# Kernel optimization log

Hardware: AMD Instinct MI355X
Metric: run time of the kernel (lower is better)

The kernel has to match this reference:

```python
import jax, jax.numpy as jnp
import numpy as np

N, D = 8192, 512


def setup_inputs() -> dict:
    key = jax.random.key(0)
    ks = jax.random.split(key, 4)
    scale = 1.0 / np.sqrt(D)
    x = jax.random.normal(ks[0], (N, D), dtype=jnp.float32)
    Wq = jax.random.normal(ks[1], (D, D), dtype=jnp.float32) * scale
    Wk = jax.random.normal(ks[2], (D, D), dtype=jnp.float32) * scale
    Wv = jax.random.normal(ks[3], (D, D), dtype=jnp.float32) * scale
    bq = jnp.zeros((D,), dtype=jnp.float32)
    bk = jnp.zeros((D,), dtype=jnp.float32)
    bv = jnp.zeros((D,), dtype=jnp.float32)
    # causal additive mask: 0 on/below diagonal, -1e9 above
    mask = jnp.where(jnp.arange(N)[:, None] >= jnp.arange(N)[None, :], 0.0, -1e9).astype(jnp.float32)
    return {"x": x, "mask": mask, "Wq": Wq, "bq": bq, "Wk": Wk, "bk": bk, "Wv": Wv, "bv": bv}


def reference(x, mask, Wq, bq, Wk, bk, Wv, bv):
    # torch Linear: y = x @ W.T + b
    q = x @ Wq.T + bq  # [N, D]
    k = x @ Wk.T + bk  # [N, D]
    v = x @ Wv.T + bv  # [N, D]
    inv_sqrt_d = 1.0 / jnp.sqrt(jnp.asarray(D, dtype=x.dtype))
    scores = q @ k.T * inv_sqrt_d + mask          # [N, N] -- the HBM-heavy intermediate
    attention = jax.nn.softmax(scores, axis=-1)   # softmax over key axis
    weighted = attention @ v                       # [N, D]
    return weighted
```

## Files before the change

kernel.cpp:

```cpp
#include <hip/hip_runtime.h>
#include <hip/hip_bf16.h>
#include <stdint.h>


#define N_TOK 8192
#define DIM   512
#define NQB   128
#define CCH   12
#define MAXCH 11
#define NCHTOT 748

typedef __attribute__((ext_vector_type(8))) short bfrag;
typedef __attribute__((ext_vector_type(4))) float facc;
typedef __attribute__((ext_vector_type(4))) unsigned short us4v;
typedef __attribute__((ext_vector_type(2))) float f32x2v;

#define MFMA16(a, b, c) __builtin_amdgcn_mfma_f32_16x16x32_bf16((a), (b), (c), 0, 0, 0)

__device__ __forceinline__ unsigned short f2bf(float f) {
    union { float f; unsigned int u; } v; v.f = f;
    unsigned int r = v.u + 0x7fffu + ((v.u >> 16) & 1u);
    return (unsigned short)(r >> 16);
}
__device__ __forceinline__ float bf2f(unsigned int bits16) {
    union { unsigned int u; float f; } v; v.u = bits16 << 16;
    return v.f;
}
__device__ __forceinline__ void cp16(const unsigned short* g, const unsigned short* l) {
    __builtin_amdgcn_global_load_lds(
        (const __attribute__((address_space(1))) void*)g,
        (__attribute__((address_space(3))) void*)l, 16, 0, 0);
}

__device__ __forceinline__ int part_idx(int qb, int c) {
    return qb + 122 * c - 6 * c * c;
}

__global__ void cvt_x_kernel(const float* __restrict__ src,
                             unsigned short* __restrict__ dst, int n4) {
    int i = blockIdx.x * blockDim.x + threadIdx.x;
    if (i >= n4) return;
    float4 v = ((const float4*)src)[i];
    us4v o; o[0] = f2bf(v.x); o[1] = f2bf(v.y); o[2] = f2bf(v.z); o[3] = f2bf(v.w);
    ((us4v*)dst)[i] = o;
}

__global__ void cvt_w_kernel(const float* __restrict__ wq,
                             const float* __restrict__ wk,
                             const float* __restrict__ wv,
                             unsigned short* __restrict__ dst) {
    int i = blockIdx.x * blockDim.x + threadIdx.x;
    int g = i >> 16;
    int o = i & 65535;
    const float* s = (g == 0) ? wq : (g == 1) ? wk : wv;
    float4 v = ((const float4*)s)[o];
    us4v p; p[0] = f2bf(v.x); p[1] = f2bf(v.y); p[2] = f2bf(v.z); p[3] = f2bf(v.w);
    ((us4v*)dst)[i] = p;
}

__global__ __launch_bounds__(512, 1) void qkv_fused(
    const unsigned short* __restrict__ xb,
    const unsigned short* __restrict__ wb,
    const float* __restrict__ biasq, const float* __restrict__ biask,
    const float* __restrict__ biasv,
    unsigned short* __restrict__ Qb, unsigned short* __restrict__ Kb,
    unsigned short* __restrict__ VTb) {
    const int bid = blockIdx.x;
    const int idx = (bid & 7) * 32 + (bid >> 3);
    const int bx = idx >> 2, by = idx & 3;
    const int r0 = bx * 128, c0 = by * 128;
    const int tid = threadIdx.x, lane = tid & 63, w = tid >> 6;
    const int wm = w >> 2, wn = w & 3;
    const int lr = lane & 15, lkc = lane >> 4;

    __shared__ unsigned short A_lds[2][128 * 64];
    __shared__ unsigned short B_lds[2][3][128 * 64];

    const int st_row = w * 8 + (lane >> 3);
    const int st_gs  = ((lane & 7) ^ (lane >> 3)) * 8;
    auto stage = [&](int step, int buf) {
        const int kb = step * 64;
#pragma unroll
        for (int i = 0; i < 2; ++i) {
            const int r = i * 64 + st_row;
            cp16(xb + (size_t)(r0 + r) * 512 + kb + st_gs,
                 &A_lds[buf][(i * 512 + w * 64) * 8]);
#pragma unroll
            for (int z = 0; z < 3; ++z)
                cp16(wb + (size_t)z * 262144 + (size_t)(c0 + r) * 512 + kb + st_gs,
                     &B_lds[buf][z][(i * 512 + w * 64) * 8]);
        }
    };

    facc acc[3][4][2] = {};
    stage(0, 0);
    __syncthreads();

    int buf = 0;
    for (int step = 0; step < 8; ++step) {
        if (step + 1 < 8) stage(step + 1, buf ^ 1);
        bfrag af[4][2];
#pragma unroll
        for (int i = 0; i < 4; ++i) {
            const int m = wm * 64 + i * 16 + lr;
            const int m7 = m & 7;
#pragma unroll
            for (int kk = 0; kk < 2; ++kk)
                af[i][kk] = *(const bfrag*)&A_lds[buf][(m * 8 + ((kk * 4 + lkc) ^ m7)) * 8];
        }
#pragma unroll
        for (int z = 0; z < 3; ++z) {
            bfrag bf[2][2];
#pragma unroll
            for (int j = 0; j < 2; ++j) {
                const int n = wn * 32 + j * 16 + lr;
                const int n7 = n & 7;
#pragma unroll
                for (int kk = 0; kk < 2; ++kk)
                    bf[j][kk] = *(const bfrag*)&B_lds[buf][z][(n * 8 + ((kk * 4 + lkc) ^ n7)) * 8];
            }
            __builtin_amdgcn_s_setprio(1);
#pragma unroll
            for (int kk = 0; kk < 2; ++kk)
#pragma unroll
                for (int i = 0; i < 4; ++i)
#pragma unroll
                    for (int j = 0; j < 2; ++j)
                        acc[z][i][j] = MFMA16(af[i][kk], bf[j][kk], acc[z][i][j]);
            __builtin_amdgcn_s_setprio(0);
        }
        __syncthreads();
        buf ^= 1;
    }

#pragma unroll
    for (int z = 0; z < 3; ++z) {
        const float* bias = (z == 0) ? biasq : (z == 1) ? biask : biasv;
        if (z < 2) {
            unsigned short* out = (z == 0) ? Qb : Kb;
#pragma unroll
            for (int i = 0; i < 4; ++i)
#pragma unroll
                for (int j = 0; j < 2; ++j) {
                    const int col = c0 + wn * 32 + j * 16 + lr;
                    const float bv_ = bias[col];
#pragma unroll
                    for (int r = 0; r < 4; ++r) {
                        const int row = r0 + wm * 64 + i * 16 + lkc * 4 + r;
                        out[(size_t)row * 512 + col] = f2bf(acc[z][i][j][r] + bv_);
                    }
                }
        } else {
#pragma unroll
            for (int i = 0; i < 4; ++i)
#pragma unroll
                for (int j = 0; j < 2; ++j) {
                    const int col = c0 + wn * 32 + j * 16 + lr;
                    const float bv_ = bias[col];
                    us4v pk;
#pragma unroll
                    for (int r = 0; r < 4; ++r) pk[r] = f2bf(acc[z][i][j][r] + bv_);
                    *(us4v*)(VTb + (size_t)col * 8192 + (r0 + wm * 64 + i * 16 + lkc * 4)) = pk;
                }
        }
    }
}

__global__ __launch_bounds__(512, 2) void attn_partial(
    const unsigned short* __restrict__ Qb, const unsigned short* __restrict__ Kb,
    const unsigned short* __restrict__ VTb,
    unsigned short* __restrict__ Opart, float* __restrict__ ml) {
    const int hb   = blockIdx.x;
    const int xcd  = hb & 7, pos = hb >> 3;
    const int idx  = (xcd < 4 ? xcd * 94 : 376 + (xcd - 4) * 93) + pos;
    int c = 0;
#pragma unroll
    for (int cc = 1; cc < MAXCH; ++cc)
        if (idx >= 134 * cc - 6 * cc * cc) c = cc;
    const int qb  = 12 * c + (idx - (134 * c - 6 * c * c));
    const int kb0 = c * CCH;
    const int kb1 = min(kb0 + CCH, qb + 1);

    const int tid  = threadIdx.x;
    const int lane = tid & 63;
    const int wv   = tid >> 6;
    const int sr   = wv & 3;
    const int ch   = wv >> 2;
    const int lr   = lane & 15;
    const int lkc  = lane >> 4;
    const int lk   = lkc * 8;
    const int qrow0 = qb * 64;

    __shared__ unsigned short Klds[2][64 * 512];
    __shared__ float          S_lds[64][65];
    __shared__ unsigned short P_lds[64][80];
    __shared__ float m_lds[64], l_lds[64], sc_lds[64];

    if (tid < 64) { m_lds[tid] = -1e30f; l_lds[tid] = 0.f; }

    auto stage_k = [&](int kb, int buf) {
        const unsigned short* src = Kb + (size_t)kb * (64 * 512) + (lane ^ wv) * 8;
#pragma unroll
        for (int i = 0; i < 8; ++i) {
            const int rl = wv + 8 * i;
            cp16(src + (size_t)rl * 512, &Klds[buf][rl * 512]);
        }
    };

    bfrag q[16];
    {
        const unsigned short* qp = Qb + (size_t)(qrow0 + sr * 16 + lr) * 512 + lk;
#pragma unroll
        for (int s = 0; s < 16; ++s) q[s] = *(const bfrag*)(qp + s * 32);
    }
    facc o[4][4] = {};
    stage_k(kb0, 0);
    __syncthreads();

    const int row = tid >> 3;
    const int sub = tid & 7;
    const float sm_scale = 0.044194173824159216f;
    int cur = 0;

    for (int kb = kb0; kb < kb1; ++kb) {
        const int cb = kb * 64;
        if (kb + 1 < kb1) stage_k(kb + 1, cur ^ 1);
        bfrag vbf[2][4];
#pragma unroll
        for (int s = 0; s < 2; ++s)
#pragma unroll
            for (int j = 0; j < 4; ++j)
                vbf[s][j] = *(const bfrag*)(VTb + (size_t)(wv * 64 + j * 16 + lr) * 8192
                                            + cb + s * 32 + lk);
#pragma unroll
        for (int tc = 0; tc < 2; ++tc) {
            facc sa0 = {}, sa1 = {};
            const int rl = ch * 32 + tc * 16 + lr;
            const unsigned short* kbase = &Klds[cur][rl * 512];
            const int rx = rl & 7;
            __builtin_amdgcn_s_setprio(1);
#pragma unroll
            for (int s = 0; s < 16; s += 2) {
                const int sl0 = (s * 4 + lkc) ^ rx;
                const int sl1 = ((s + 1) * 4 + lkc) ^ rx;
                sa0 = MFMA16(q[s],     *(const bfrag*)(kbase + sl0 * 8), sa0);
                sa1 = MFMA16(q[s + 1], *(const bfrag*)(kbase + sl1 * 8), sa1);
            }
            __builtin_amdgcn_s_setprio(0);
#pragma unroll
            for (int r = 0; r < 4; ++r)
                S_lds[sr * 16 + lkc * 4 + r][ch * 32 + tc * 16 + lr] = sa0[r] + sa1[r];
        }
        __syncthreads();

        {
            const int grow  = qrow0 + row;
            const bool diag = (kb == qb);
            float sv[8];
#pragma unroll
            for (int j = 0; j < 8; ++j) {
                float v = S_lds[row][sub * 8 + j] * sm_scale;
                if (diag && (cb + sub * 8 + j > grow)) v = -1e30f;
                sv[j] = v;
            }
            float mx = sv[0];
#pragma unroll
            for (int j = 1; j < 8; ++j) mx = fmaxf(mx, sv[j]);
            mx = fmaxf(mx, __shfl_xor(mx, 1));
            mx = fmaxf(mx, __shfl_xor(mx, 2));
            mx = fmaxf(mx, __shfl_xor(mx, 4));
            const float m_old = m_lds[row];
            const float m_new = fmaxf(m_old, mx);
            float sum = 0.f;
            bfrag pv_;
#pragma unroll
            for (int j = 0; j < 8; ++j) {
                float p = __expf(sv[j] - m_new);
                sum += p;
                pv_[j] = (short)f2bf(p);
            }
            sum += __shfl_xor(sum, 1);
            sum += __shfl_xor(sum, 2);
            sum += __shfl_xor(sum, 4);
            if (sub == 0) {
                const float scl = __expf(m_old - m_new);
                sc_lds[row] = scl;
                m_lds[row]  = m_new;
                l_lds[row]  = l_lds[row] * scl + sum;
            }
            *(bfrag*)(&P_lds[row][sub * 8]) = pv_;
        }
        __syncthreads();

#pragma unroll
        for (int i = 0; i < 4; ++i) {
            float s0 = sc_lds[i * 16 + lkc * 4 + 0];
            float s1 = sc_lds[i * 16 + lkc * 4 + 1];
            float s2 = sc_lds[i * 16 + lkc * 4 + 2];
            float s3 = sc_lds[i * 16 + lkc * 4 + 3];
#pragma unroll
            for (int j = 0; j < 4; ++j) {
                o[i][j][0] *= s0; o[i][j][1] *= s1;
                o[i][j][2] *= s2; o[i][j][3] *= s3;
            }
        }
#pragma unroll
        for (int s = 0; s < 2; ++s) {
            bfrag pa[4];
#pragma unroll
            for (int i = 0; i < 4; ++i)
                pa[i] = *(const bfrag*)(&P_lds[i * 16 + lr][s * 32 + lk]);
            __builtin_amdgcn_s_setprio(1);
#pragma unroll
            for (int i = 0; i < 4; ++i)
#pragma unroll
                for (int j = 0; j < 4; ++j)
                    o[i][j] = MFMA16(pa[i], vbf[s][j], o[i][j]);
            __builtin_amdgcn_s_setprio(0);
        }
        cur ^= 1;
    }

    {
        const size_t obase = (size_t)idx * (64 * 512);
#pragma unroll
        for (int i = 0; i < 4; ++i)
#pragma unroll
            for (int j = 0; j < 4; ++j) {
                const int colb = wv * 64 + j * 16 + lr;
#pragma unroll
                for (int r = 0; r < 4; ++r) {
                    const int rrow = i * 16 + lkc * 4 + r;
                    Opart[obase + (size_t)rrow * 512 + colb] = f2bf(o[i][j][r]);
                }
            }
        if (tid < 64) {
            ml[(size_t)idx * 128 + tid * 2 + 0] = m_lds[tid];
            ml[(size_t)idx * 128 + tid * 2 + 1] = l_lds[tid];
        }
    }
}

__global__ __launch_bounds__(256) void combine_k(
    const unsigned short* __restrict__ Opart, const float* __restrict__ ml,
    float* __restrict__ out) {
    const int qb  = blockIdx.x;
    const int rg  = blockIdx.y;
    const int nch = qb / 12 + 1;
    const int tid = threadIdx.x;
    __shared__ float wts[MAXCH][8];

    if (tid < 8) {
        const int lrow = rg * 8 + tid;
        float M = -1e30f;
        for (int cc = 0; cc < nch; ++cc)
            M = fmaxf(M, ml[(size_t)part_idx(qb, cc) * 128 + lrow * 2]);
        float den = 0.f;
        for (int cc = 0; cc < nch; ++cc) {
            float mc = ml[(size_t)part_idx(qb, cc) * 128 + lrow * 2];
            float lc = ml[(size_t)part_idx(qb, cc) * 128 + lrow * 2 + 1];
            den += lc * __expf(mc - M);
        }
        const float inv = 1.f / den;
#pragma unroll
        for (int cc = 0; cc < MAXCH; ++cc)
            wts[cc][tid] = (cc < nch)
                ? __expf(ml[(size_t)part_idx(qb, cc) * 128 + lrow * 2] - M) * inv
                : 0.f;
    }
    __syncthreads();

    float a0[8] = {}, a1[8] = {};
#pragma unroll
    for (int cc = 0; cc < MAXCH; ++cc) {
        const size_t base = (size_t)part_idx(qb, cc) * (64 * 512);
#pragma unroll
        for (int r = 0; r < 8; ++r) {
            const unsigned int pk = *(const unsigned int*)(
                Opart + base + (size_t)(rg * 8 + r) * 512 + tid * 2);
            const float w = wts[cc][r];
            a0[r] += w * bf2f(pk & 0xffffu);
            a1[r] += w * bf2f(pk >> 16);
        }
    }
#pragma unroll
    for (int r = 0; r < 8; ++r) {
        f32x2v res; res[0] = a0[r]; res[1] = a1[r];
        *(f32x2v*)(out + (size_t)(qb * 64 + rg * 8 + r) * 512 + tid * 2) = res;
    }
}

extern "C" void kernel_launch(void* const* d_in, const int* in_sizes, int n_in,
                              void* d_out, int out_size, void* d_ws, size_t ws_size,
                              hipStream_t stream) {
    const float* x  = (const float*)d_in[0];
    const float* Wq = (const float*)d_in[2];
    const float* bq = (const float*)d_in[3];
    const float* Wk = (const float*)d_in[4];
    const float* bk = (const float*)d_in[5];
    const float* Wv = (const float*)d_in[6];
    const float* bv = (const float*)d_in[7];
    float* out = (float*)d_out;

    char* ws = (char*)d_ws;
    unsigned short* xb  = (unsigned short*)(ws);
    unsigned short* Wb  = (unsigned short*)(ws + 8388608);
    unsigned short* Qb  = (unsigned short*)(ws + 9961472);
    unsigned short* Kb  = (unsigned short*)(ws + 18350080);
    unsigned short* VTb = (unsigned short*)(ws + 26738688);
    unsigned short* Op  = (unsigned short*)(ws + 35127296);
    float*          mlp = (float*)(ws + 84148224);

    hipLaunchKernelGGL(cvt_x_kernel, dim3(4096), dim3(256), 0, stream, x, xb, 1048576);
    hipLaunchKernelGGL(cvt_w_kernel, dim3(768), dim3(256), 0, stream, Wq, Wk, Wv, Wb);
    hipLaunchKernelGGL(qkv_fused, dim3(256), dim3(512), 0, stream,
                       xb, Wb, bq, bk, bv, Qb, Kb, VTb);
    hipLaunchKernelGGL(attn_partial, dim3(NCHTOT), dim3(512), 0, stream,
                       Qb, Kb, VTb, Op, mlp);
    hipLaunchKernelGGL(combine_k, dim3(NQB, 8), dim3(256), 0, stream, Op, mlp, out);
}
```

Baseline: 518.9 us.

## Replace syncthreads with targeted waitcnt barriers and deepen QKV load pipeline

Swaps __syncthreads for inline-asm barriers that wait only on the needed counters (lgkmcnt or vmcnt), so async global-to-LDS copies can stay in flight across barriers. The QKV GEMM prefetches two stages ahead with a vmcnt(8) wait, and biases are hoisted into registers. The attention kernel issues the next K stage after the V loads, shrinks the P_lds padding and drops the s_setprio hints. The hand-written vmcnt counts and the out-of-range refetch of stage 7 are fragile, and the barriers may let LDS reads race with the in-flight copies.

```diff
diff --git a/kernel.cpp b/kernel.cpp
--- a/kernel.cpp
+++ b/kernel.cpp
@@ -16,6 +16,11 @@
 typedef __attribute__((ext_vector_type(2))) float f32x2v;
 
 #define MFMA16(a, b, c) __builtin_amdgcn_mfma_f32_16x16x32_bf16((a), (b), (c), 0, 0, 0)
+
+#define BAR_LGKM() asm volatile("s_waitcnt lgkmcnt(0)\ns_barrier" ::: "memory")
+#define BAR_VMALL() asm volatile("s_waitcnt vmcnt(0) lgkmcnt(0)\ns_barrier" ::: "memory")
+#define BAR_VM0()  asm volatile("s_waitcnt vmcnt(0)\ns_barrier" ::: "memory")
+#define BAR_VM8()  asm volatile("s_waitcnt vmcnt(8)\ns_barrier" ::: "memory")
 
 __device__ __forceinline__ unsigned short f2bf(float f) {
     union { float f; unsigned int u; } v; v.f = f;
@@ -76,6 +81,15 @@
     __shared__ unsigned short A_lds[2][128 * 64];
     __shared__ unsigned short B_lds[2][3][128 * 64];
 
+    float bias_r[3][2];
+#pragma unroll
+    for (int j = 0; j < 2; ++j) {
+        const int col = c0 + wn * 32 + j * 16 + lr;
+        bias_r[0][j] = biasq[col];
+        bias_r[1][j] = biask[col];
+        bias_r[2][j] = biasv[col];
+    }
+
     const int st_row = w * 8 + (lane >> 3);
     const int st_gs  = ((lane & 7) ^ (lane >> 3)) * 8;
     auto stage = [&](int step, int buf) {
@@ -94,11 +108,11 @@
 
     facc acc[3][4][2] = {};
     stage(0, 0);
-    __syncthreads();
-
-    int buf = 0;
-    for (int step = 0; step < 8; ++step) {
-        if (step + 1 < 8) stage(step + 1, buf ^ 1);
+    stage(1, 1);
+    BAR_VM8();
+
+    for (int t = 0; t < 8; ++t) {
+        const int b = t & 1;
         bfrag af[4][2];
 #pragma unroll
         for (int i = 0; i < 4; ++i) {
@@ -106,7 +120,7 @@
             const int m7 = m & 7;
 #pragma unroll
             for (int kk = 0; kk < 2; ++kk)
-                af[i][kk] = *(const bfrag*)&A_lds[buf][(m * 8 + ((kk * 4 + lkc) ^ m7)) * 8];
+                af[i][kk] = *(const bfrag*)&A_lds[b][(m * 8 + ((kk * 4 + lkc) ^ m7)) * 8];
         }
 #pragma unroll
         for (int z = 0; z < 3; ++z) {
@@ -117,9 +131,8 @@
                 const int n7 = n & 7;
 #pragma unroll
                 for (int kk = 0; kk < 2; ++kk)
-                    bf[j][kk] = *(const bfrag*)&B_lds[buf][z][(n * 8 + ((kk * 4 + lkc) ^ n7)) * 8];
-            }
-            __builtin_amdgcn_s_setprio(1);
+                    bf[j][kk] = *(const bfrag*)&B_lds[b][z][(n * 8 + ((kk * 4 + lkc) ^ n7)) * 8];
+            }
 #pragma unroll
             for (int kk = 0; kk < 2; ++kk)
 #pragma unroll
@@ -127,15 +140,14 @@
 #pragma unroll
                     for (int j = 0; j < 2; ++j)
                         acc[z][i][j] = MFMA16(af[i][kk], bf[j][kk], acc[z][i][j]);
-            __builtin_amdgcn_s_setprio(0);
-        }
-        __syncthreads();
-        buf ^= 1;
+        }
+        BAR_LGKM();
+        stage(min(t + 2, 7), b);
+        BAR_VM8();
     }
 
 #pragma unroll
     for (int z = 0; z < 3; ++z) {
-        const float* bias = (z == 0) ? biasq : (z == 1) ? biask : biasv;
         if (z < 2) {
             unsigned short* out = (z == 0) ? Qb : Kb;
 #pragma unroll
@@ -143,7 +155,7 @@
 #pragma unroll
                 for (int j = 0; j < 2; ++j) {
                     const int col = c0 + wn * 32 + j * 16 + lr;
-                    const float bv_ = bias[col];
+                    const float bv_ = bias_r[z][j];
 #pragma unroll
                     for (int r = 0; r < 4; ++r) {
                         const int row = r0 + wm * 64 + i * 16 + lkc * 4 + r;
@@ -156,7 +168,7 @@
 #pragma unroll
                 for (int j = 0; j < 2; ++j) {
                     const int col = c0 + wn * 32 + j * 16 + lr;
-                    const float bv_ = bias[col];
+                    const float bv_ = bias_r[z][j];
                     us4v pk;
 #pragma unroll
                     for (int r = 0; r < 4; ++r) pk[r] = f2bf(acc[z][i][j][r] + bv_);
@@ -193,7 +205,7 @@
 
     __shared__ unsigned short Klds[2][64 * 512];
     __shared__ float          S_lds[64][65];
-    __shared__ unsigned short P_lds[64][80];
+    __shared__ unsigned short P_lds[64][72];
     __shared__ float m_lds[64], l_lds[64], sc_lds[64];
 
     if (tid < 64) { m_lds[tid] = -1e30f; l_lds[tid] = 0.f; }
@@ -215,7 +227,7 @@
     }
     facc o[4][4] = {};
     stage_k(kb0, 0);
-    __syncthreads();
+    BAR_VMALL();
 
     const int row = tid >> 3;
     const int sub = tid & 7;
@@ -224,7 +236,6 @@
 
     for (int kb = kb0; kb < kb1; ++kb) {
         const int cb = kb * 64;
-        if (kb + 1 < kb1) stage_k(kb + 1, cur ^ 1);
         bfrag vbf[2][4];
 #pragma unroll
         for (int s = 0; s < 2; ++s)
@@ -232,13 +243,14 @@
             for (int j = 0; j < 4; ++j)
                 vbf[s][j] = *(const bfrag*)(VTb + (size_t)(wv * 64 + j * 16 + lr) * 8192
                                             + cb + s * 32 + lk);
+        if (kb + 1 < kb1) stage_k(kb + 1, cur ^ 1);
+
 #pragma unroll
         for (int tc = 0; tc < 2; ++tc) {
             facc sa0 = {}, sa1 = {};
             const int rl = ch * 32 + tc * 16 + lr;
             const unsigned short* kbase = &Klds[cur][rl * 512];
             const int rx = rl & 7;
-            __builtin_amdgcn_s_setprio(1);
 #pragma unroll
             for (int s = 0; s < 16; s += 2) {
                 const int sl0 = (s * 4 + lkc) ^ rx;
@@ -246,12 +258,11 @@
                 sa0 = MFMA16(q[s],     *(const bfrag*)(kbase + sl0 * 8), sa0);
                 sa1 = MFMA16(q[s + 1], *(const bfrag*)(kbase + sl1 * 8), sa1);
             }
-            __builtin_amdgcn_s_setprio(0);
 #pragma unroll
             for (int r = 0; r < 4; ++r)
                 S_lds[sr * 16 + lkc * 4 + r][ch * 32 + tc * 16 + lr] = sa0[r] + sa1[r];
         }
-        __syncthreads();
+        BAR_LGKM();
 
         {
             const int grow  = qrow0 + row;
@@ -290,7 +301,7 @@
             }
             *(bfrag*)(&P_lds[row][sub * 8]) = pv_;
         }
-        __syncthreads();
+        BAR_LGKM();
 
 #pragma unroll
         for (int i = 0; i < 4; ++i) {
@@ -310,14 +321,13 @@
 #pragma unroll
             for (int i = 0; i < 4; ++i)
                 pa[i] = *(const bfrag*)(&P_lds[i * 16 + lr][s * 32 + lk]);
-            __builtin_amdgcn_s_setprio(1);
 #pragma unroll
             for (int i = 0; i < 4; ++i)
 #pragma unroll
                 for (int j = 0; j < 4; ++j)
                     o[i][j] = MFMA16(pa[i], vbf[s][j], o[i][j]);
-            __builtin_amdgcn_s_setprio(0);
-        }
+        }
+        BAR_VM0();
         cur ^= 1;
     }
 
```

Result: slower. 532.4 us (+2.6%).
